# Performance work log

Hardware: AMD Instinct MI355X
Metric: run time of the kernel (lower is better)

Reference implementation:

```python
import jax, jax.numpy as jnp
import numpy as np

N_NODES = 100000
DIM_IN = 128
DIM_OUT = 128
N_EDGES = 1600000
EPS = 0.0  # PyG GINConv default, non-trainable


def setup_inputs() -> dict:
    key = jax.random.key(0)
    k1, k2, k3, k4, k5, k6 = jax.random.split(key, 6)
    node_feature = jax.random.normal(k1, (N_NODES, DIM_IN), dtype=jnp.float32)
    edge_index = jax.random.randint(k2, (2, N_EDGES), 0, N_NODES, dtype=jnp.int64)
    s1 = 1.0 / np.sqrt(DIM_IN)
    s2 = 1.0 / np.sqrt(DIM_OUT)
    W1 = jax.random.uniform(k3, (DIM_IN, DIM_OUT), jnp.float32, -s1, s1)
    b1 = jax.random.uniform(k4, (DIM_OUT,), jnp.float32, -s1, s1)
    W2 = jax.random.uniform(k5, (DIM_OUT, DIM_OUT), jnp.float32, -s2, s2)
    b2 = jax.random.uniform(k6, (DIM_OUT,), jnp.float32, -s2, s2)
    return {"node_feature": node_feature, "edge_index": edge_index,
            "W1": W1, "b1": b1, "W2": W2, "b2": b2}


def reference(node_feature, edge_index, W1, b1, W2, b2):
    src, dst = edge_index[0], edge_index[1]
    # scatter-add neighbor aggregation: messages x_j = x[src] summed at dst
    agg = jax.ops.segment_sum(node_feature[src], dst, num_segments=N_NODES)  # [N, d]
    h = (1.0 + EPS) * node_feature + agg
    h = jax.nn.relu(h @ W1 + b1)
    return h @ W2 + b2
```

## Files before the change

### kernel.cpp

```cpp
#include <hip/hip_runtime.h>

#define NN 100000
#define D  128
#define NE 1600000

#define NBK2 782
#define CAP2 2816
#define EPB  8192
#define NFB  196
#define ENTCAP 2048

typedef __bf16 bf16x8 __attribute__((ext_vector_type(8)));
typedef __bf16 bf16x4 __attribute__((ext_vector_type(4)));
typedef float  f32x4  __attribute__((ext_vector_type(4)));

__global__ void xprep_kernel(const float* __restrict__ x, __bf16* __restrict__ xb) {
    int i = blockIdx.x * 256 + threadIdx.x;
    if (i < NN * 32) {
        float4 v = reinterpret_cast<const float4*>(x)[i];
        bf16x4 o = {(__bf16)v.x, (__bf16)v.y, (__bf16)v.z, (__bf16)v.w};
        reinterpret_cast<bf16x4*>(xb)[i] = o;
    }
}

__global__ void wprep_kernel(const float* __restrict__ W1, const float* __restrict__ W2,
                             __bf16* __restrict__ w1t, __bf16* __restrict__ w2t) {
    int i = blockIdx.x * 256 + threadIdx.x;
    if (i < 16384) {
        int c = i >> 7, k = i & 127;
        w1t[i] = (__bf16)W1[k * 128 + c];
    } else if (i < 32768) {
        int j = i - 16384;
        int c = j >> 7, k = j & 127;
        w2t[j] = (__bf16)W2[k * 128 + c];
    }
}

__global__ void zero_gcur_kernel(int* __restrict__ gcur) {
    int i = blockIdx.x * 256 + threadIdx.x;
    if (i < NBK2) gcur[i] = 0;
}

__global__ __launch_bounds__(512)
void fill2_kernel(const int* __restrict__ ei, int* __restrict__ gcur,
                  int* __restrict__ bedge) {
    __shared__ int            stage[EPB];
    __shared__ unsigned short bid16[EPB];
    __shared__ int            lofs[NBK2];
    __shared__ int            lpos[NBK2];
    __shared__ int            gbase[NBK2];
    __shared__ int            ssum[512];
    __shared__ int            tot;

    const int tid = threadIdx.x;
    const int e0  = blockIdx.x * EPB;

    for (int b = tid; b < NBK2; b += 512) lpos[b] = 0;
    __syncthreads();

    int eb[16], epk[16];
    #pragma unroll 16
    for (int k = 0; k < 16; ++k) {
        int e = e0 + k * 512 + tid;
        eb[k] = -1;
        if (e < NE) {
            int s = ei[e];
            int d = ei[NE + e];
            if ((unsigned)s < NN && (unsigned)d < NN) {
                eb[k]  = d >> 7;
                epk[k] = ((d & 127) << 17) | s;
                atomicAdd(&lpos[eb[k]], 1);
            }
        }
    }
    __syncthreads();

    int t2 = tid * 2;
    int c0 = (t2 < NBK2) ? lpos[t2] : 0;
    int c1 = (t2 + 1 < NBK2) ? lpos[t2 + 1] : 0;
    ssum[tid] = c0 + c1;
    __syncthreads();
    for (int off = 1; off < 512; off <<= 1) {
        int v = (tid >= off) ? ssum[tid - off] : 0;
        __syncthreads();
        ssum[tid] += v;
        __syncthreads();
    }
    int excl = ssum[tid] - (c0 + c1);
    if (t2 < NBK2) {
        lofs[t2] = excl;
        lpos[t2] = excl;
        if (c0) gbase[t2] = atomicAdd(&gcur[t2], c0);
    }
    if (t2 + 1 < NBK2) {
        lofs[t2 + 1] = excl + c0;
        lpos[t2 + 1] = excl + c0;
        if (c1) gbase[t2 + 1] = atomicAdd(&gcur[t2 + 1], c1);
    }
    if (tid == 511) tot = ssum[511];
    __syncthreads();

    #pragma unroll 16
    for (int k = 0; k < 16; ++k) {
        if (eb[k] >= 0) {
            int r = atomicAdd(&lpos[eb[k]], 1);
            stage[r] = epk[k];
            bid16[r] = (unsigned short)eb[k];
        }
    }
    __syncthreads();

    int T = tot;
    for (int i = tid; i < T; i += 512) {
        int b   = bid16[i];
        int pos = gbase[b] + (i - lofs[b]);
        if (pos < CAP2) bedge[b * CAP2 + pos] = stage[i];
    }
}

__global__ __launch_bounds__(256)
void gather3_kernel(const __bf16* __restrict__ xb, const int* __restrict__ gcur,
                    const int* __restrict__ bedge, __bf16* __restrict__ hb) {
    __shared__ int ent[ENTCAP];
    __shared__ int c64[64], ofs[65], cur[64], scn[64];

    const int b    = blockIdx.x >> 1;
    const int half = blockIdx.x & 1;
    const int tid  = threadIdx.x;

    int cnt = gcur[b]; if (cnt > CAP2) cnt = CAP2;
    const int base = b * CAP2;

    if (tid < 64) c64[tid] = 0;
    __syncthreads();

    for (int i = tid; i < cnt; i += 256) {
        int v  = bedge[base + i];
        int dl = v >> 17;
        if ((dl >> 6) == half) atomicAdd(&c64[dl & 63], 1);
    }
    __syncthreads();

    if (tid < 64) scn[tid] = c64[tid];
    __syncthreads();
    #pragma unroll
    for (int off = 1; off < 64; off <<= 1) {
        int v = (tid >= off && tid < 64) ? scn[tid - off] : 0;
        __syncthreads();
        if (tid < 64) scn[tid] += v;
        __syncthreads();
    }
    if (tid < 64) {
        ofs[tid + 1] = scn[tid];
        if (tid == 0) ofs[0] = 0;
        cur[tid] = scn[tid] - c64[tid];
    }
    __syncthreads();

    for (int i = tid; i < cnt; i += 256) {
        int v  = bedge[base + i];
        int dl = v >> 17;
        if ((dl >> 6) == half) {
            int r = atomicAdd(&cur[dl & 63], 1);
            if (r < ENTCAP) ent[r] = v & 0x1FFFF;
        }
    }
    __syncthreads();

    const int wave   = tid >> 6;
    const int lane   = tid & 63;
    const int half32 = lane >> 5;
    const int l31    = lane & 31;
    const bf16x4* xv4 = reinterpret_cast<const bf16x4*>(xb);

    for (int q = wave; q < 64; q += 4) {
        int node = b * 128 + half * 64 + q;
        if (node >= NN) continue;
        int beg = ofs[q], end = ofs[q + 1];
        if (beg > ENTCAP) beg = ENTCAP;
        if (end > ENTCAP) end = ENTCAP;

        float a0 = 0.f, a1 = 0.f, a2 = 0.f, a3 = 0.f;
        float b0 = 0.f, b1 = 0.f, b2f = 0.f, b3 = 0.f;
        int j = beg;
        for (; j + 4 <= end; j += 4) {
            int s0 = ent[j + half32];
            int s1 = ent[j + 2 + half32];
            bf16x4 v0 = xv4[(size_t)s0 * 32 + l31];
            bf16x4 v1 = xv4[(size_t)s1 * 32 + l31];
            a0 += (float)v0[0]; a1 += (float)v0[1];
            a2 += (float)v0[2]; a3 += (float)v0[3];
            b0 += (float)v1[0]; b1 += (float)v1[1];
            b2f += (float)v1[2]; b3 += (float)v1[3];
        }
        if (j + 2 <= end) {
            int s0 = ent[j + half32];
            bf16x4 v0 = xv4[(size_t)s0 * 32 + l31];
            a0 += (float)v0[0]; a1 += (float)v0[1];
            a2 += (float)v0[2]; a3 += (float)v0[3];
            j += 2;
        }
        if (j < end && half32 == 0) {
            int s0 = ent[j];
            bf16x4 v0 = xv4[(size_t)s0 * 32 + l31];
            a0 += (float)v0[0]; a1 += (float)v0[1];
            a2 += (float)v0[2]; a3 += (float)v0[3];
        }
        a0 += b0; a1 += b1; a2 += b2f; a3 += b3;
        a0 += __shfl_xor(a0, 32); a1 += __shfl_xor(a1, 32);
        a2 += __shfl_xor(a2, 32); a3 += __shfl_xor(a3, 32);

        if (half32 == 0) {
            bf16x4 sv = xv4[(size_t)node * 32 + l31];
            bf16x4 o = {(__bf16)(a0 + (float)sv[0]), (__bf16)(a1 + (float)sv[1]),
                        (__bf16)(a2 + (float)sv[2]), (__bf16)(a3 + (float)sv[3])};
            reinterpret_cast<bf16x4*>(hb)[(size_t)node * 32 + l31] = o;
        }
    }
}

__global__ __launch_bounds__(256)
void mlp_mfma_kernel(const __bf16* __restrict__ hb,
                     const __bf16* __restrict__ w1t,
                     const __bf16* __restrict__ w2t,
                     const float* __restrict__ b1,
                     const float* __restrict__ b2,
                     float* __restrict__ out) {
    __shared__ __align__(16) unsigned char sh_h[64 * 256];
    __shared__ __align__(16) unsigned char sh_w[128 * 256];

    const int tid   = threadIdx.x;
    const int wv    = tid >> 6;
    const int lane  = tid & 63;
    const int l15   = lane & 15;
    const int kbyte = (lane >> 4) * 16;
    const int row0  = blockIdx.x * 64;

    for (int c = tid; c < 1024; c += 256) {
        int r = c >> 4, s = c & 15;
        int grow = row0 + r;
        int4 val = make_int4(0, 0, 0, 0);
        if (grow < NN) val = *reinterpret_cast<const int4*>(hb + (size_t)grow * 128 + s * 8);
        *reinterpret_cast<int4*>(sh_h + r * 256 + ((s * 16) ^ ((r & 7) << 4))) = val;
    }
    for (int c = tid; c < 2048; c += 256) {
        int r = c >> 4, s = c & 15;
        int4 val = *reinterpret_cast<const int4*>(w1t + r * 128 + s * 8);
        *reinterpret_cast<int4*>(sh_w + r * 256 + ((s * 16) ^ ((r & 7) << 4))) = val;
    }
    __syncthreads();

    bf16x8 bf1[2][4];
    #pragma unroll
    for (int nn = 0; nn < 2; ++nn) {
        int col = wv * 32 + nn * 16 + l15;
        #pragma unroll
        for (int ks = 0; ks < 4; ++ks)
            bf1[nn][ks] = *reinterpret_cast<const bf16x8*>(
                sh_w + col * 256 + ((ks * 64 + kbyte) ^ ((col & 7) << 4)));
    }

    f32x4 acc[4][2];
    #pragma unroll
    for (int m = 0; m < 4; ++m) {
        acc[m][0] = f32x4{0.f, 0.f, 0.f, 0.f};
        acc[m][1] = f32x4{0.f, 0.f, 0.f, 0.f};
        int row = m * 16 + l15;
        bf16x8 af[4];
        #pragma unroll
        for (int ks = 0; ks < 4; ++ks)
            af[ks] = *reinterpret_cast<const bf16x8*>(
                sh_h + row * 256 + ((ks * 64 + kbyte) ^ ((row & 7) << 4)));
        #pragma unroll
        for (int ks = 0; ks < 4; ++ks) {
            acc[m][0] = __builtin_amdgcn_mfma_f32_16x16x32_bf16(af[ks], bf1[0][ks], acc[m][0], 0, 0, 0);
            acc[m][1] = __builtin_amdgcn_mfma_f32_16x16x32_bf16(af[ks], bf1[1][ks], acc[m][1], 0, 0, 0);
        }
    }

    float bias1a = b1[wv * 32 + l15];
    float bias1b = b1[wv * 32 + 16 + l15];

    __syncthreads();

    #pragma unroll
    for (int m = 0; m < 4; ++m) {
        #pragma unroll
        for (int nn = 0; nn < 2; ++nn) {
            int col = wv * 32 + nn * 16 + l15;
            float bb = nn ? bias1b : bias1a;
            #pragma unroll
            for (int j = 0; j < 4; ++j) {
                int row = m * 16 + (lane >> 4) * 4 + j;
                float v = fmaxf(acc[m][nn][j] + bb, 0.f);
                *reinterpret_cast<__bf16*>(
                    sh_h + row * 256 + ((col * 2) ^ ((row & 7) << 4))) = (__bf16)v;
            }
        }
    }
    for (int c = tid; c < 2048; c += 256) {
        int r = c >> 4, s = c & 15;
        int4 val = *reinterpret_cast<const int4*>(w2t + r * 128 + s * 8);
        *reinterpret_cast<int4*>(sh_w + r * 256 + ((s * 16) ^ ((r & 7) << 4))) = val;
    }
    __syncthreads();

    bf16x8 bf2[2][4];
    #pragma unroll
    for (int nn = 0; nn < 2; ++nn) {
        int col = wv * 32 + nn * 16 + l15;
        #pragma unroll
        for (int ks = 0; ks < 4; ++ks)
            bf2[nn][ks] = *reinterpret_cast<const bf16x8*>(
                sh_w + col * 256 + ((ks * 64 + kbyte) ^ ((col & 7) << 4)));
    }

    f32x4 acc2[4][2];
    #pragma unroll
    for (int m = 0; m < 4; ++m) {
        acc2[m][0] = f32x4{0.f, 0.f, 0.f, 0.f};
        acc2[m][1] = f32x4{0.f, 0.f, 0.f, 0.f};
        int row = m * 16 + l15;
        bf16x8 af[4];
        #pragma unroll
        for (int ks = 0; ks < 4; ++ks)
            af[ks] = *reinterpret_cast<const bf16x8*>(
                sh_h + row * 256 + ((ks * 64 + kbyte) ^ ((row & 7) << 4)));
        #pragma unroll
        for (int ks = 0; ks < 4; ++ks) {
            acc2[m][0] = __builtin_amdgcn_mfma_f32_16x16x32_bf16(af[ks], bf2[0][ks], acc2[m][0], 0, 0, 0);
            acc2[m][1] = __builtin_amdgcn_mfma_f32_16x16x32_bf16(af[ks], bf2[1][ks], acc2[m][1], 0, 0, 0);
        }
    }

    float bias2a = b2[wv * 32 + l15];
    float bias2b = b2[wv * 32 + 16 + l15];
    #pragma unroll
    for (int m = 0; m < 4; ++m) {
        #pragma unroll
        for (int nn = 0; nn < 2; ++nn) {
            int col = wv * 32 + nn * 16 + l15;
            float bb = nn ? bias2b : bias2a;
            #pragma unroll
            for (int j = 0; j < 4; ++j) {
                int row = row0 + m * 16 + (lane >> 4) * 4 + j;
                if (row < NN) out[(size_t)row * 128 + col] = acc2[m][nn][j] + bb;
            }
        }
    }
}

extern "C" void kernel_launch(void* const* d_in, const int* in_sizes, int n_in,
                              void* d_out, int out_size, void* d_ws, size_t ws_size,
                              hipStream_t stream) {
    const float* x  = (const float*)d_in[0];
    const int*   ei = (const int*)d_in[1];
    const float* W1 = (const float*)d_in[2];
    const float* b1 = (const float*)d_in[3];
    const float* W2 = (const float*)d_in[4];
    const float* b2 = (const float*)d_in[5];
    float* out = (float*)d_out;

    int* gcur  = (int*)d_ws;
    int* bedge = gcur + NBK2;
    size_t int_end = (size_t)(NBK2 + (size_t)NBK2 * CAP2) * 4;
    size_t bf_off  = (int_end + 255) & ~(size_t)255;
    __bf16* xb  = (__bf16*)((char*)d_ws + bf_off);
    __bf16* hb  = xb + (size_t)NN * D;
    __bf16* w1t = hb + (size_t)NN * D;
    __bf16* w2t = w1t + D * D;

    xprep_kernel<<<(NN * 32 + 255) / 256, 256, 0, stream>>>(x, xb);
    wprep_kernel<<<128, 256, 0, stream>>>(W1, W2, w1t, w2t);
    zero_gcur_kernel<<<(NBK2 + 255) / 256, 256, 0, stream>>>(gcur);

    fill2_kernel<<<NFB, 512, 0, stream>>>(ei, gcur, bedge);
    gather3_kernel<<<NBK2 * 2, 256, 0, stream>>>(xb, gcur, bedge, hb);

    mlp_mfma_kernel<<<(NN + 63) / 64, 256, 0, stream>>>(hb, w1t, w2t, b1, b2, out);
}
```

Before: 134.9 us.

## Fuse neighbor gather with MLP in one kernel per 128-node bucket

Merges the gather kernel and the MFMA MLP kernel into a single 512-thread kernel that aggregates 128 destination nodes straight into shared memory and then runs both GEMMs from there. This drops the bf16 intermediate h buffer round-trip through global memory and one kernel launch. Weight fragments are now read directly from global or L2 instead of being staged in shared memory. The fill kernel also halves edges per block, doubling its grid. Fewer blocks (782) with heavier per-block work may reduce occupancy and load balance.

```diff
diff --git a/kernel.cpp b/kernel.cpp
--- a/kernel.cpp
+++ b/kernel.cpp
@@ -6,9 +6,8 @@
 
 #define NBK2 782
 #define CAP2 2816
-#define EPB  8192
-#define NFB  196
-#define ENTCAP 2048
+#define EPB  4096
+#define NFB  391
 
 typedef __bf16 bf16x8 __attribute__((ext_vector_type(8)));
 typedef __bf16 bf16x4 __attribute__((ext_vector_type(4)));
@@ -58,9 +57,9 @@
     for (int b = tid; b < NBK2; b += 512) lpos[b] = 0;
     __syncthreads();
 
-    int eb[16], epk[16];
-    #pragma unroll 16
-    for (int k = 0; k < 16; ++k) {
+    int eb[8], epk[8];
+    #pragma unroll 8
+    for (int k = 0; k < 8; ++k) {
         int e = e0 + k * 512 + tid;
         eb[k] = -1;
         if (e < NE) {
@@ -100,8 +99,8 @@
     if (tid == 511) tot = ssum[511];
     __syncthreads();
 
-    #pragma unroll 16
-    for (int k = 0; k < 16; ++k) {
+    #pragma unroll 8
+    for (int k = 0; k < 8; ++k) {
         if (eb[k] >= 0) {
             int r = atomicAdd(&lpos[eb[k]], 1);
             stage[r] = epk[k];
@@ -118,52 +117,51 @@
     }
 }
 
-__global__ __launch_bounds__(256)
-void gather3_kernel(const __bf16* __restrict__ xb, const int* __restrict__ gcur,
-                    const int* __restrict__ bedge, __bf16* __restrict__ hb) {
-    __shared__ int ent[ENTCAP];
-    __shared__ int c64[64], ofs[65], cur[64], scn[64];
-
-    const int b    = blockIdx.x >> 1;
-    const int half = blockIdx.x & 1;
-    const int tid  = threadIdx.x;
-
+__global__ __launch_bounds__(512)
+void fused_gather_mlp_kernel(const __bf16* __restrict__ xb,
+                             const int* __restrict__ gcur,
+                             const int* __restrict__ bedge,
+                             const __bf16* __restrict__ w1t,
+                             const __bf16* __restrict__ w2t,
+                             const float* __restrict__ b1,
+                             const float* __restrict__ b2,
+                             float* __restrict__ out) {
+    __shared__ __align__(16) unsigned char sh_h[128 * 256];
+    __shared__ int ent[CAP2];
+    __shared__ int c128[128], cur[128], scn[128], ofs[129];
+
+    const int b   = blockIdx.x;
+    const int tid = threadIdx.x;
     int cnt = gcur[b]; if (cnt > CAP2) cnt = CAP2;
     const int base = b * CAP2;
 
-    if (tid < 64) c64[tid] = 0;
-    __syncthreads();
-
-    for (int i = tid; i < cnt; i += 256) {
-        int v  = bedge[base + i];
-        int dl = v >> 17;
-        if ((dl >> 6) == half) atomicAdd(&c64[dl & 63], 1);
-    }
-    __syncthreads();
-
-    if (tid < 64) scn[tid] = c64[tid];
-    __syncthreads();
-    #pragma unroll
-    for (int off = 1; off < 64; off <<= 1) {
-        int v = (tid >= off && tid < 64) ? scn[tid - off] : 0;
+    if (tid < 128) c128[tid] = 0;
+    __syncthreads();
+    for (int i = tid; i < cnt; i += 512) {
+        int v = bedge[base + i];
+        atomicAdd(&c128[v >> 17], 1);
+    }
+    __syncthreads();
+    int c = (tid < 128) ? c128[tid] : 0;
+    if (tid < 128) scn[tid] = c;
+    __syncthreads();
+    #pragma unroll
+    for (int off = 1; off < 128; off <<= 1) {
+        int v = (tid >= off && tid < 128) ? scn[tid - off] : 0;
         __syncthreads();
-        if (tid < 64) scn[tid] += v;
+        if (tid < 128) scn[tid] += v;
         __syncthreads();
     }
-    if (tid < 64) {
+    if (tid < 128) {
         ofs[tid + 1] = scn[tid];
         if (tid == 0) ofs[0] = 0;
-        cur[tid] = scn[tid] - c64[tid];
-    }
-    __syncthreads();
-
-    for (int i = tid; i < cnt; i += 256) {
-        int v  = bedge[base + i];
-        int dl = v >> 17;
-        if ((dl >> 6) == half) {
-            int r = atomicAdd(&cur[dl & 63], 1);
-            if (r < ENTCAP) ent[r] = v & 0x1FFFF;
-        }
+        cur[tid] = scn[tid] - c;
+    }
+    __syncthreads();
+    for (int i = tid; i < cnt; i += 512) {
+        int v = bedge[base + i];
+        int r = atomicAdd(&cur[v >> 17], 1);
+        ent[r] = v & 0x1FFFF;
     }
     __syncthreads();
 
@@ -173,91 +171,67 @@
     const int l31    = lane & 31;
     const bf16x4* xv4 = reinterpret_cast<const bf16x4*>(xb);
 
-    for (int q = wave; q < 64; q += 4) {
-        int node = b * 128 + half * 64 + q;
-        if (node >= NN) continue;
-        int beg = ofs[q], end = ofs[q + 1];
-        if (beg > ENTCAP) beg = ENTCAP;
-        if (end > ENTCAP) end = ENTCAP;
-
+    for (int q = wave; q < 128; q += 8) {
+        int node = b * 128 + q;
         float a0 = 0.f, a1 = 0.f, a2 = 0.f, a3 = 0.f;
-        float b0 = 0.f, b1 = 0.f, b2f = 0.f, b3 = 0.f;
-        int j = beg;
-        for (; j + 4 <= end; j += 4) {
-            int s0 = ent[j + half32];
-            int s1 = ent[j + 2 + half32];
-            bf16x4 v0 = xv4[(size_t)s0 * 32 + l31];
-            bf16x4 v1 = xv4[(size_t)s1 * 32 + l31];
-            a0 += (float)v0[0]; a1 += (float)v0[1];
-            a2 += (float)v0[2]; a3 += (float)v0[3];
-            b0 += (float)v1[0]; b1 += (float)v1[1];
-            b2f += (float)v1[2]; b3 += (float)v1[3];
-        }
-        if (j + 2 <= end) {
-            int s0 = ent[j + half32];
-            bf16x4 v0 = xv4[(size_t)s0 * 32 + l31];
-            a0 += (float)v0[0]; a1 += (float)v0[1];
-            a2 += (float)v0[2]; a3 += (float)v0[3];
-            j += 2;
-        }
-        if (j < end && half32 == 0) {
-            int s0 = ent[j];
-            bf16x4 v0 = xv4[(size_t)s0 * 32 + l31];
-            a0 += (float)v0[0]; a1 += (float)v0[1];
-            a2 += (float)v0[2]; a3 += (float)v0[3];
-        }
-        a0 += b0; a1 += b1; a2 += b2f; a3 += b3;
-        a0 += __shfl_xor(a0, 32); a1 += __shfl_xor(a1, 32);
-        a2 += __shfl_xor(a2, 32); a3 += __shfl_xor(a3, 32);
-
+        if (node < NN) {
+            int beg = ofs[q], end = ofs[q + 1];
+            float b0 = 0.f, b1f = 0.f, b2f = 0.f, b3f = 0.f;
+            int j = beg;
+            for (; j + 4 <= end; j += 4) {
+                int s0 = ent[j + half32];
+                int s1 = ent[j + 2 + half32];
+                bf16x4 v0 = xv4[(size_t)s0 * 32 + l31];
+                bf16x4 v1 = xv4[(size_t)s1 * 32 + l31];
+                a0 += (float)v0[0]; a1 += (float)v0[1];
+                a2 += (float)v0[2]; a3 += (float)v0[3];
+                b0 += (float)v1[0]; b1f += (float)v1[1];
+                b2f += (float)v1[2]; b3f += (float)v1[3];
+            }
+            if (j + 2 <= end) {
+                int s0 = ent[j + half32];
+                bf16x4 v0 = xv4[(size_t)s0 * 32 + l31];
+                a0 += (float)v0[0]; a1 += (float)v0[1];
+                a2 += (float)v0[2]; a3 += (float)v0[3];
+                j += 2;
+            }
+            if (j < end && half32 == 0) {
+                int s0 = ent[j];
+                bf16x4 v0 = xv4[(size_t)s0 * 32 + l31];
+                a0 += (float)v0[0]; a1 += (float)v0[1];
+                a2 += (float)v0[2]; a3 += (float)v0[3];
+            }
+            a0 += b0; a1 += b1f; a2 += b2f; a3 += b3f;
+            a0 += __shfl_xor(a0, 32); a1 += __shfl_xor(a1, 32);
+            a2 += __shfl_xor(a2, 32); a3 += __shfl_xor(a3, 32);
+            if (half32 == 0) {
+                bf16x4 sv = xv4[(size_t)node * 32 + l31];
+                a0 += (float)sv[0]; a1 += (float)sv[1];
+                a2 += (float)sv[2]; a3 += (float)sv[3];
+            }
+        }
         if (half32 == 0) {
-            bf16x4 sv = xv4[(size_t)node * 32 + l31];
-            bf16x4 o = {(__bf16)(a0 + (float)sv[0]), (__bf16)(a1 + (float)sv[1]),
-                        (__bf16)(a2 + (float)sv[2]), (__bf16)(a3 + (float)sv[3])};
-            reinterpret_cast<bf16x4*>(hb)[(size_t)node * 32 + l31] = o;
-        }
-    }
-}
-
-__global__ __launch_bounds__(256)
-void mlp_mfma_kernel(const __bf16* __restrict__ hb,
-                     const __bf16* __restrict__ w1t,
-                     const __bf16* __restrict__ w2t,
-                     const float* __restrict__ b1,
-                     const float* __restrict__ b2,
-                     float* __restrict__ out) {
-    __shared__ __align__(16) unsigned char sh_h[64 * 256];
-    __shared__ __align__(16) unsigned char sh_w[128 * 256];
-
-    const int tid   = threadIdx.x;
-    const int wv    = tid >> 6;
-    const int lane  = tid & 63;
+            bf16x4 o = {(__bf16)a0, (__bf16)a1, (__bf16)a2, (__bf16)a3};
+            *reinterpret_cast<bf16x4*>(
+                sh_h + q * 256 + ((l31 * 8) ^ ((q & 7) << 4))) = o;
+        }
+    }
+    __syncthreads();
+
+    const int wr    = wave >> 2;
+    const int wc    = wave & 3;
     const int l15   = lane & 15;
     const int kbyte = (lane >> 4) * 16;
-    const int row0  = blockIdx.x * 64;
-
-    for (int c = tid; c < 1024; c += 256) {
-        int r = c >> 4, s = c & 15;
-        int grow = row0 + r;
-        int4 val = make_int4(0, 0, 0, 0);
-        if (grow < NN) val = *reinterpret_cast<const int4*>(hb + (size_t)grow * 128 + s * 8);
-        *reinterpret_cast<int4*>(sh_h + r * 256 + ((s * 16) ^ ((r & 7) << 4))) = val;
-    }
-    for (int c = tid; c < 2048; c += 256) {
-        int r = c >> 4, s = c & 15;
-        int4 val = *reinterpret_cast<const int4*>(w1t + r * 128 + s * 8);
-        *reinterpret_cast<int4*>(sh_w + r * 256 + ((s * 16) ^ ((r & 7) << 4))) = val;
-    }
-    __syncthreads();
-
-    bf16x8 bf1[2][4];
+    const int kelem = (lane >> 4) * 8;
+
+    bf16x8 bf[2][4];
     #pragma unroll
     for (int nn = 0; nn < 2; ++nn) {
-        int col = wv * 32 + nn * 16 + l15;
+        int col = wc * 32 + nn * 16 + l15;
         #pragma unroll
         for (int ks = 0; ks < 4; ++ks)
-            bf1[nn][ks] = *reinterpret_cast<const bf16x8*>(
-                sh_w + col * 256 + ((ks * 64 + kbyte) ^ ((col & 7) << 4)));
+            bf[nn][ks] = *reinterpret_cast<const bf16x8*>(
+                w1t + col * 128 + ks * 32 + kelem);
     }
 
     f32x4 acc[4][2];
@@ -265,7 +239,7 @@
     for (int m = 0; m < 4; ++m) {
         acc[m][0] = f32x4{0.f, 0.f, 0.f, 0.f};
         acc[m][1] = f32x4{0.f, 0.f, 0.f, 0.f};
-        int row = m * 16 + l15;
+        int row = wr * 64 + m * 16 + l15;
         bf16x8 af[4];
         #pragma unroll
         for (int ks = 0; ks < 4; ++ks)
@@ -273,13 +247,13 @@
                 sh_h + row * 256 + ((ks * 64 + kbyte) ^ ((row & 7) << 4)));
         #pragma unroll
         for (int ks = 0; ks < 4; ++ks) {
-            acc[m][0] = __builtin_amdgcn_mfma_f32_16x16x32_bf16(af[ks], bf1[0][ks], acc[m][0], 0, 0, 0);
-            acc[m][1] = __builtin_amdgcn_mfma_f32_16x16x32_bf16(af[ks], bf1[1][ks], acc[m][1], 0, 0, 0);
-        }
-    }
-
-    float bias1a = b1[wv * 32 + l15];
-    float bias1b = b1[wv * 32 + 16 + l15];
+            acc[m][0] = __builtin_amdgcn_mfma_f32_16x16x32_bf16(af[ks], bf[0][ks], acc[m][0], 0, 0, 0);
+            acc[m][1] = __builtin_amdgcn_mfma_f32_16x16x32_bf16(af[ks], bf[1][ks], acc[m][1], 0, 0, 0);
+        }
+    }
+
+    float bias1a = b1[wc * 32 + l15];
+    float bias1b = b1[wc * 32 + 16 + l15];
 
     __syncthreads();
 
@@ -287,32 +261,26 @@
     for (int m = 0; m < 4; ++m) {
         #pragma unroll
         for (int nn = 0; nn < 2; ++nn) {
-            int col = wv * 32 + nn * 16 + l15;
+            int col = wc * 32 + nn * 16 + l15;
             float bb = nn ? bias1b : bias1a;
             #pragma unroll
             for (int j = 0; j < 4; ++j) {
-                int row = m * 16 + (lane >> 4) * 4 + j;
+                int row = wr * 64 + m * 16 + (lane >> 4) * 4 + j;
                 float v = fmaxf(acc[m][nn][j] + bb, 0.f);
                 *reinterpret_cast<__bf16*>(
                     sh_h + row * 256 + ((col * 2) ^ ((row & 7) << 4))) = (__bf16)v;
             }
         }
     }
-    for (int c = tid; c < 2048; c += 256) {
-        int r = c >> 4, s = c & 15;
-        int4 val = *reinterpret_cast<const int4*>(w2t + r * 128 + s * 8);
-        *reinterpret_cast<int4*>(sh_w + r * 256 + ((s * 16) ^ ((r & 7) << 4))) = val;
-    }
-    __syncthreads();
-
-    bf16x8 bf2[2][4];
+    __syncthreads();
+
     #pragma unroll
     for (int nn = 0; nn < 2; ++nn) {
-        int col = wv * 32 + nn * 16 + l15;
+        int col = wc * 32 + nn * 16 + l15;
         #pragma unroll
         for (int ks = 0; ks < 4; ++ks)
-            bf2[nn][ks] = *reinterpret_cast<const bf16x8*>(
-                sh_w + col * 256 + ((ks * 64 + kbyte) ^ ((col & 7) << 4)));
+            bf[nn][ks] = *reinterpret_cast<const bf16x8*>(
+                w2t + col * 128 + ks * 32 + kelem);
     }
 
     f32x4 acc2[4][2];
@@ -320,7 +288,7 @@
     for (int m = 0; m < 4; ++m) {
         acc2[m][0] = f32x4{0.f, 0.f, 0.f, 0.f};
         acc2[m][1] = f32x4{0.f, 0.f, 0.f, 0.f};
-        int row = m * 16 + l15;
+        int row = wr * 64 + m * 16 + l15;
         bf16x8 af[4];
         #pragma unroll
         for (int ks = 0; ks < 4; ++ks)
@@ -328,22 +296,22 @@
                 sh_h + row * 256 + ((ks * 64 + kbyte) ^ ((row & 7) << 4)));
         #pragma unroll
         for (int ks = 0; ks < 4; ++ks) {
-            acc2[m][0] = __builtin_amdgcn_mfma_f32_16x16x32_bf16(af[ks], bf2[0][ks], acc2[m][0], 0, 0, 0);
-            acc2[m][1] = __builtin_amdgcn_mfma_f32_16x16x32_bf16(af[ks], bf2[1][ks], acc2[m][1], 0, 0, 0);
-        }
-    }
-
-    float bias2a = b2[wv * 32 + l15];
-    float bias2b = b2[wv * 32 + 16 + l15];
+            acc2[m][0] = __builtin_amdgcn_mfma_f32_16x16x32_bf16(af[ks], bf[0][ks], acc2[m][0], 0, 0, 0);
+            acc2[m][1] = __builtin_amdgcn_mfma_f32_16x16x32_bf16(af[ks], bf[1][ks], acc2[m][1], 0, 0, 0);
+        }
+    }
+
+    float bias2a = b2[wc * 32 + l15];
+    float bias2b = b2[wc * 32 + 16 + l15];
     #pragma unroll
     for (int m = 0; m < 4; ++m) {
         #pragma unroll
         for (int nn = 0; nn < 2; ++nn) {
-            int col = wv * 32 + nn * 16 + l15;
+            int col = wc * 32 + nn * 16 + l15;
             float bb = nn ? bias2b : bias2a;
             #pragma unroll
             for (int j = 0; j < 4; ++j) {
-                int row = row0 + m * 16 + (lane >> 4) * 4 + j;
+                int row = b * 128 + wr * 64 + m * 16 + (lane >> 4) * 4 + j;
                 if (row < NN) out[(size_t)row * 128 + col] = acc2[m][nn][j] + bb;
             }
         }
@@ -366,8 +334,7 @@
     size_t int_end = (size_t)(NBK2 + (size_t)NBK2 * CAP2) * 4;
     size_t bf_off  = (int_end + 255) & ~(size_t)255;
     __bf16* xb  = (__bf16*)((char*)d_ws + bf_off);
-    __bf16* hb  = xb + (size_t)NN * D;
-    __bf16* w1t = hb + (size_t)NN * D;
+    __bf16* w1t = xb + (size_t)NN * D;
     __bf16* w2t = w1t + D * D;
 
     xprep_kernel<<<(NN * 32 + 255) / 256, 256, 0, stream>>>(x, xb);
@@ -375,7 +342,7 @@
     zero_gcur_kernel<<<(NBK2 + 255) / 256, 256, 0, stream>>>(gcur);
 
     fill2_kernel<<<NFB, 512, 0, stream>>>(ei, gcur, bedge);
-    gather3_kernel<<<NBK2 * 2, 256, 0, stream>>>(xb, gcur, bedge, hb);
-
-    mlp_mfma_kernel<<<(NN + 63) / 64, 256, 0, stream>>>(hb, w1t, w2t, b1, b2, out);
-}
+
+    fused_gather_mlp_kernel<<<NBK2, 512, 0, stream>>>(xb, gcur, bedge,
+                                                      w1t, w2t, b1, b2, out);
+}
```

New measurement: 162.0 us. 1.2x slower.
